# Performance work log

Measured on AMD Instinct MI355X. Metric: run time of the kernel, lower is better.

## Reference

```python
import jax, jax.numpy as jnp
import numpy as np

D_MODEL = 1024
NUM_HEADS = 16
D_K = D_MODEL // NUM_HEADS
CLAMP = 1e9
EPS = 1e-12


def setup_inputs() -> dict:
    key = jax.random.key(0)
    ks = jax.random.split(key, 11)
    B, S, D = 4, 2048, D_MODEL
    std = 1.0 / np.sqrt(D)
    inp = {
        'Q': jax.random.normal(ks[0], (B, S, D), jnp.float32),
        'K': jax.random.normal(ks[1], (B, S, D), jnp.float32),
        'V': jax.random.normal(ks[2], (B, S, D), jnp.float32),
        'Wq': jax.random.normal(ks[3], (D, D), jnp.float32) * std,
        'bq': jnp.zeros((D,), jnp.float32),
        'Wk': jax.random.normal(ks[4], (D, D), jnp.float32) * std,
        'bk': jnp.zeros((D,), jnp.float32),
        'Wv': jax.random.normal(ks[5], (D, D), jnp.float32) * std,
        'bv': jnp.zeros((D,), jnp.float32),
        'Wo': jax.random.normal(ks[6], (D, D), jnp.float32) * std,
        'bo': jnp.zeros((D,), jnp.float32),
    }
    return inp


def _split_heads(x):
    b, s, _ = x.shape
    return x.reshape(b, s, NUM_HEADS, D_K).transpose(0, 2, 1, 3)  # [b,h,s,dk]


def reference(Q, K, V, Wq, bq, Wk, bk, Wv, bv, Wo, bo):
    Qh = _split_heads(Q @ Wq.T + bq)
    Kh = _split_heads(K @ Wk.T + bk)
    Vh = _split_heads(V @ Wv.T + bv)
    scale = jnp.sqrt(jnp.asarray(D_K, Qh.dtype))
    scores = jnp.einsum('bhqd,bhkd->bhqk', Qh, Kh) / scale
    scores = scores - jnp.max(scores, axis=-1, keepdims=True)
    scores = jnp.clip(scores, -CLAMP, CLAMP)
    attn = jax.nn.softmax(scores, axis=-1)
    attn = jnp.clip(attn, EPS, None)
    attn = attn / jnp.sum(attn, axis=-1, keepdims=True)
    ctx = jnp.einsum('bhqk,bhkd->bhqd', attn, Vh)
    b, h, s, dk = ctx.shape
    ctx = ctx.transpose(0, 2, 1, 3).reshape(b, s, D_MODEL)
    return ctx @ Wo.T + bo
```

## Files before the change

### kernel.cpp

```cpp
#include <hip/hip_runtime.h>
#include <hip/hip_bf16.h>


typedef float  f32x4  __attribute__((ext_vector_type(4)));
typedef __bf16 bf16x8 __attribute__((ext_vector_type(8)));
typedef short  s16x8  __attribute__((ext_vector_type(8)));

#define MFMA16(a,b,c) __builtin_amdgcn_mfma_f32_16x16x32_bf16((a),(b),(c),0,0,0)

__device__ __forceinline__ unsigned short f2bf(float f) {
    union { float f; unsigned u; } v; v.f = f;
    unsigned r = v.u + 0x7fffu + ((v.u >> 16) & 1u);
    return (unsigned short)(r >> 16);
}

__device__ __forceinline__ s16x8 cvt8(const float* __restrict__ p) {
    f32x4 x = *(const f32x4*)p;
    f32x4 y = *(const f32x4*)(p + 4);
    s16x8 r;
    r[0] = (short)f2bf(x[0]); r[1] = (short)f2bf(x[1]);
    r[2] = (short)f2bf(x[2]); r[3] = (short)f2bf(x[3]);
    r[4] = (short)f2bf(y[0]); r[5] = (short)f2bf(y[1]);
    r[6] = (short)f2bf(y[2]); r[7] = (short)f2bf(y[3]);
    return r;
}

__device__ __forceinline__ void gl_lds16(const void* g, void* l) {
    __builtin_amdgcn_global_load_lds(
        (const __attribute__((address_space(1))) unsigned int*)g,
        (__attribute__((address_space(3))) unsigned int*)l, 16, 0, 0);
}

__global__ __launch_bounds__(256) void cvt_kernel(
    const float* __restrict__ src, unsigned short* __restrict__ dst, int n8)
{
    int i = blockIdx.x * 256 + threadIdx.x;
    if (i < n8) *(s16x8*)(dst + (size_t)i * 8) = cvt8(src + (size_t)i * 8);
}

template <int MODE>
__global__ __launch_bounds__(256) void gemm_bf16(
    const unsigned short* __restrict__ A,
    const unsigned short* __restrict__ W,
    const float* __restrict__ bias,
    void* __restrict__ Cv)
{
    constexpr int K = 1024;
    __shared__ unsigned short Ash[128 * 32];
    __shared__ unsigned short Bsh[128 * 32];

    const int t    = threadIdx.x;
    const int w    = t >> 6;
    const int lane = t & 63;
    const int wm   = w >> 1, wn = w & 1;
    const int lr   = lane & 15, quad = lane >> 4;

    const int m0 = blockIdx.y * 128;
    const int n0 = blockIdx.x * 128;

    const int srow = t >> 2;
    const int skp  = (t & 3) * 8;

    const unsigned short* Ap0 = A + (size_t)(m0 + srow) * K + skp;
    const unsigned short* Ap1 = Ap0 + (size_t)64 * K;
    const unsigned short* Wp0 = W + (size_t)(n0 + srow) * K + skp;
    const unsigned short* Wp1 = Wp0 + (size_t)64 * K;
    unsigned short* lA0 = &Ash[w * 512];
    unsigned short* lA1 = &Ash[2048 + w * 512];
    unsigned short* lB0 = &Bsh[w * 512];
    unsigned short* lB1 = &Bsh[2048 + w * 512];

    f32x4 acc[4][4] = {};

    for (int k0 = 0; k0 < K; k0 += 32) {
        __syncthreads();
        gl_lds16(Ap0 + k0, lA0);
        gl_lds16(Ap1 + k0, lA1);
        gl_lds16(Wp0 + k0, lB0);
        gl_lds16(Wp1 + k0, lB1);
        __syncthreads();

        bf16x8 af[4], bw[4];
#pragma unroll
        for (int i = 0; i < 4; i++)
            af[i] = *(const bf16x8*)&Ash[(wm * 64 + i * 16 + lr) * 32 + quad * 8];
#pragma unroll
        for (int j = 0; j < 4; j++)
            bw[j] = *(const bf16x8*)&Bsh[(wn * 64 + j * 16 + lr) * 32 + quad * 8];

#pragma unroll
        for (int i = 0; i < 4; i++)
#pragma unroll
            for (int j = 0; j < 4; j++)
                acc[i][j] = MFMA16(af[i], bw[j], acc[i][j]);
    }

#pragma unroll
    for (int i = 0; i < 4; i++) {
#pragma unroll
        for (int j = 0; j < 4; j++) {
            const int n = n0 + wn * 64 + j * 16 + lr;
#pragma unroll
            for (int r = 0; r < 4; r++) {
                const int m = m0 + wm * 64 + i * 16 + quad * 4 + r;
                float val = acc[i][j][r] + ((MODE == 2) ? bias[m] : bias[n]);
                if (MODE == 0) {
                    const int b = m >> 11, s = m & 2047, h = n >> 6, d = n & 63;
                    ((unsigned short*)Cv)[(((size_t)(b * 16 + h) * 2048 + s) << 6) + d] = f2bf(val);
                } else if (MODE == 1) {
                    ((float*)Cv)[(size_t)m * 1024 + n] = val;
                } else {
                    const int h = m >> 6, d = m & 63, b = n >> 11, s = n & 2047;
                    ((unsigned short*)Cv)[((size_t)(b * 16 + h) * 64 + d) * 2048 + s] = f2bf(val);
                }
            }
        }
    }
}

__global__ __launch_bounds__(256) void attn_kernel(
    const unsigned short* __restrict__ Qh,
    const unsigned short* __restrict__ Kh,
    const unsigned short* __restrict__ Vt,
    unsigned short* __restrict__ ctx)
{
    constexpr int KS = 72;
    __shared__ unsigned short Ksh[64 * KS];
    __shared__ unsigned short Vts[64 * KS];
    __shared__ unsigned short Psh[4][16 * KS];

    const int t    = threadIdx.x;
    const int w    = t >> 6;
    const int lane = t & 63;
    const int lr   = lane & 15, quad = lane >> 4;

    const int bh = blockIdx.y, qblk = blockIdx.x;
    const size_t base = (size_t)bh * 2048 * 64;
    const unsigned short* Qp = Qh + base;
    const unsigned short* Kg = Kh + base + (size_t)lane * 64 + w * 16;
    const unsigned short* Vg = Vt + base + (size_t)lane * 2048 + w * 16;

    const int q0 = qblk * 64 + w * 16;
    bf16x8 aq0 = *(const bf16x8*)(Qp + (size_t)(q0 + lr) * 64 + quad * 8);
    bf16x8 aq1 = *(const bf16x8*)(Qp + (size_t)(q0 + lr) * 64 + 32 + quad * 8);

    f32x4 Of[4] = {};
    float lsum[4] = {0.f, 0.f, 0.f, 0.f};

    for (int kb = 0; kb < 2048; kb += 64) {
        s16x8 kv0 = *(const s16x8*)(Kg + (size_t)kb * 64);
        s16x8 kv1 = *(const s16x8*)(Kg + (size_t)kb * 64 + 8);
        s16x8 vv0 = *(const s16x8*)(Vg + kb);
        s16x8 vv1 = *(const s16x8*)(Vg + kb + 8);

        __syncthreads();
        *(s16x8*)&Ksh[lane * KS + w * 16]     = kv0;
        *(s16x8*)&Ksh[lane * KS + w * 16 + 8] = kv1;
        *(s16x8*)&Vts[lane * KS + w * 16]     = vv0;
        *(s16x8*)&Vts[lane * KS + w * 16 + 8] = vv1;
        __syncthreads();

        f32x4 sc[4];
#pragma unroll
        for (int nt = 0; nt < 4; nt++) {
            const unsigned short* kr = &Ksh[(16 * nt + lr) * KS + quad * 8];
            f32x4 c = {};
            c = MFMA16(aq0, *(const bf16x8*)kr, c);
            c = MFMA16(aq1, *(const bf16x8*)(kr + 32), c);
            sc[nt] = c;
        }

#pragma unroll
        for (int r = 0; r < 4; r++) {
            float p0 = __expf(sc[0][r] * 0.125f);
            float p1 = __expf(sc[1][r] * 0.125f);
            float p2 = __expf(sc[2][r] * 0.125f);
            float p3 = __expf(sc[3][r] * 0.125f);
            lsum[r] += (p0 + p1) + (p2 + p3);
            unsigned short* pr = &Psh[w][(quad * 4 + r) * KS + lr];
            pr[0]  = f2bf(p0);
            pr[16] = f2bf(p1);
            pr[32] = f2bf(p2);
            pr[48] = f2bf(p3);
        }
        __asm__ __volatile__("s_waitcnt lgkmcnt(0)" ::: "memory");

        bf16x8 pf0 = *(const bf16x8*)&Psh[w][lr * KS + quad * 8];
        bf16x8 pf1 = *(const bf16x8*)&Psh[w][lr * KS + 32 + quad * 8];
#pragma unroll
        for (int dt = 0; dt < 4; dt++) {
            const unsigned short* vr = &Vts[(dt * 16 + lr) * KS + quad * 8];
            Of[dt] = MFMA16(pf0, *(const bf16x8*)vr, Of[dt]);
            Of[dt] = MFMA16(pf1, *(const bf16x8*)(vr + 32), Of[dt]);
        }
    }

    const int b = bh >> 4, h = bh & 15;
#pragma unroll
    for (int r = 0; r < 4; r++) {
        float l = lsum[r];
        l += __shfl_xor(l, 1);
        l += __shfl_xor(l, 2);
        l += __shfl_xor(l, 4);
        l += __shfl_xor(l, 8);
        const float inv = 1.0f / l;
        const int q = q0 + quad * 4 + r;
        unsigned short* cp = ctx + ((size_t)b * 2048 + q) * 1024 + h * 64;
#pragma unroll
        for (int dt = 0; dt < 4; dt++)
            cp[dt * 16 + lr] = f2bf(Of[dt][r] * inv);
    }
}

extern "C" void kernel_launch(void* const* d_in, const int* in_sizes, int n_in,
                              void* d_out, int out_size, void* d_ws, size_t ws_size,
                              hipStream_t stream) {
    const float* Q  = (const float*)d_in[0];
    const float* K  = (const float*)d_in[1];
    const float* V  = (const float*)d_in[2];
    const float* Wq = (const float*)d_in[3];
    const float* bq = (const float*)d_in[4];
    const float* Wk = (const float*)d_in[5];
    const float* bk = (const float*)d_in[6];
    const float* Wv = (const float*)d_in[7];
    const float* bv = (const float*)d_in[8];
    const float* Wo = (const float*)d_in[9];
    const float* bo = (const float*)d_in[10];

    const size_t EB = (size_t)8192 * 1024;
    const size_t EW = (size_t)1024 * 1024;
    unsigned short* Xb  = (unsigned short*)d_ws;
    unsigned short* Wqb = Xb  + EB;
    unsigned short* Wkb = Wqb + EW;
    unsigned short* Wvb = Wkb + EW;
    unsigned short* Wob = Wvb + EW;
    unsigned short* Qh  = Wob + EW;
    unsigned short* Kh  = Qh  + EB;
    unsigned short* Vtw = Kh  + EB;
    unsigned short* Ctx = Xb;

    const int n8b = (int)(EB / 8);
    const int n8w = (int)(EW / 8);

    cvt_kernel<<<n8w / 256, 256, 0, stream>>>(Wq, Wqb, n8w);
    cvt_kernel<<<n8w / 256, 256, 0, stream>>>(Wk, Wkb, n8w);
    cvt_kernel<<<n8w / 256, 256, 0, stream>>>(Wv, Wvb, n8w);
    cvt_kernel<<<n8w / 256, 256, 0, stream>>>(Wo, Wob, n8w);

    dim3 tb(256), gP(8, 64), gT(64, 8);

    cvt_kernel<<<n8b / 256, 256, 0, stream>>>(Q, Xb, n8b);
    gemm_bf16<0><<<gP, tb, 0, stream>>>(Xb, Wqb, bq, Qh);

    cvt_kernel<<<n8b / 256, 256, 0, stream>>>(K, Xb, n8b);
    gemm_bf16<0><<<gP, tb, 0, stream>>>(Xb, Wkb, bk, Kh);

    cvt_kernel<<<n8b / 256, 256, 0, stream>>>(V, Xb, n8b);
    gemm_bf16<2><<<gT, tb, 0, stream>>>(Wvb, Xb, bv, Vtw);

    attn_kernel<<<dim3(32, 64), tb, 0, stream>>>(Qh, Kh, Vtw, Ctx);

    gemm_bf16<1><<<gP, tb, 0, stream>>>(Ctx, Wob, bo, (float*)d_out);
}
```

Measured before the change: 435.3 us.

## Keep softmax probabilities in registers via transposed QK MFMA and permlane swaps

Swaps the operand order of the QK^T MFMA so the score tile comes out transposed, with each lane holding scores for a single query across keys. The probabilities are then packed to bf16 with v_cvt_pk_bf16_f32 and rearranged with permlane32/16 swaps into the A-operand layout for the PV MFMA. This removes the per-wave LDS round trip for P (bf16 stores, waitcnt, reloads) and the manual bf16 rounding. Row sums are reduced with cross-quad shuffles and broadcast at the end. It relies on gfx950-specific instructions and on the permlane mapping being correct.

```diff
diff --git a/kernel.cpp b/kernel.cpp
--- a/kernel.cpp
+++ b/kernel.cpp
@@ -5,6 +5,7 @@
 typedef float  f32x4  __attribute__((ext_vector_type(4)));
 typedef __bf16 bf16x8 __attribute__((ext_vector_type(8)));
 typedef short  s16x8  __attribute__((ext_vector_type(8)));
+typedef int    i32x4  __attribute__((ext_vector_type(4)));
 
 #define MFMA16(a,b,c) __builtin_amdgcn_mfma_f32_16x16x32_bf16((a),(b),(c),0,0,0)
 
@@ -29,6 +30,18 @@
     __builtin_amdgcn_global_load_lds(
         (const __attribute__((address_space(1))) unsigned int*)g,
         (__attribute__((address_space(3))) unsigned int*)l, 16, 0, 0);
+}
+
+__device__ __forceinline__ int cvtpk_bf16(float lo, float hi) {
+    int r;
+    asm("v_cvt_pk_bf16_f32 %0, %1, %2" : "=v"(r) : "v"(lo), "v"(hi));
+    return r;
+}
+__device__ __forceinline__ void plswap32(int& a, int& b) {
+    asm("v_permlane32_swap_b32 %0, %1" : "+v"(a), "+v"(b));
+}
+__device__ __forceinline__ void plswap16(int& a, int& b) {
+    asm("v_permlane16_swap_b32 %0, %1" : "+v"(a), "+v"(b));
 }
 
 __global__ __launch_bounds__(256) void cvt_kernel(
@@ -127,7 +140,6 @@
     constexpr int KS = 72;
     __shared__ unsigned short Ksh[64 * KS];
     __shared__ unsigned short Vts[64 * KS];
-    __shared__ unsigned short Psh[4][16 * KS];
 
     const int t    = threadIdx.x;
     const int w    = t >> 6;
@@ -145,7 +157,7 @@
     bf16x8 aq1 = *(const bf16x8*)(Qp + (size_t)(q0 + lr) * 64 + 32 + quad * 8);
 
     f32x4 Of[4] = {};
-    float lsum[4] = {0.f, 0.f, 0.f, 0.f};
+    float lsum = 0.f;
 
     for (int kb = 0; kb < 2048; kb += 64) {
         s16x8 kv0 = *(const s16x8*)(Kg + (size_t)kb * 64);
@@ -160,33 +172,39 @@
         *(s16x8*)&Vts[lane * KS + w * 16 + 8] = vv1;
         __syncthreads();
 
-        f32x4 sc[4];
+        f32x4 pe[4];
 #pragma unroll
         for (int nt = 0; nt < 4; nt++) {
             const unsigned short* kr = &Ksh[(16 * nt + lr) * KS + quad * 8];
             f32x4 c = {};
-            c = MFMA16(aq0, *(const bf16x8*)kr, c);
-            c = MFMA16(aq1, *(const bf16x8*)(kr + 32), c);
-            sc[nt] = c;
+            c = MFMA16(*(const bf16x8*)kr, aq0, c);
+            c = MFMA16(*(const bf16x8*)(kr + 32), aq1, c);
+            f32x4 p;
+#pragma unroll
+            for (int r = 0; r < 4; r++) p[r] = __expf(c[r] * 0.125f);
+            lsum += (p[0] + p[1]) + (p[2] + p[3]);
+            pe[nt] = p;
         }
 
-#pragma unroll
-        for (int r = 0; r < 4; r++) {
-            float p0 = __expf(sc[0][r] * 0.125f);
-            float p1 = __expf(sc[1][r] * 0.125f);
-            float p2 = __expf(sc[2][r] * 0.125f);
-            float p3 = __expf(sc[3][r] * 0.125f);
-            lsum[r] += (p0 + p1) + (p2 + p3);
-            unsigned short* pr = &Psh[w][(quad * 4 + r) * KS + lr];
-            pr[0]  = f2bf(p0);
-            pr[16] = f2bf(p1);
-            pr[32] = f2bf(p2);
-            pr[48] = f2bf(p3);
-        }
-        __asm__ __volatile__("s_waitcnt lgkmcnt(0)" ::: "memory");
-
-        bf16x8 pf0 = *(const bf16x8*)&Psh[w][lr * KS + quad * 8];
-        bf16x8 pf1 = *(const bf16x8*)&Psh[w][lr * KS + 32 + quad * 8];
+        int a0 = cvtpk_bf16(pe[0][0], pe[0][1]);
+        int a1 = cvtpk_bf16(pe[0][2], pe[0][3]);
+        int b0 = cvtpk_bf16(pe[1][0], pe[1][1]);
+        int b1 = cvtpk_bf16(pe[1][2], pe[1][3]);
+        plswap32(a0, b0); plswap32(a1, b1);
+        plswap16(a0, b0); plswap16(a1, b1);
+        i32x4 f0; f0[0] = a0; f0[1] = a1; f0[2] = b0; f0[3] = b1;
+
+        int c0 = cvtpk_bf16(pe[2][0], pe[2][1]);
+        int c1 = cvtpk_bf16(pe[2][2], pe[2][3]);
+        int d0 = cvtpk_bf16(pe[3][0], pe[3][1]);
+        int d1 = cvtpk_bf16(pe[3][2], pe[3][3]);
+        plswap32(c0, d0); plswap32(c1, d1);
+        plswap16(c0, d0); plswap16(c1, d1);
+        i32x4 f1; f1[0] = c0; f1[1] = c1; f1[2] = d0; f1[3] = d1;
+
+        bf16x8 pf0 = __builtin_bit_cast(bf16x8, f0);
+        bf16x8 pf1 = __builtin_bit_cast(bf16x8, f1);
+
 #pragma unroll
         for (int dt = 0; dt < 4; dt++) {
             const unsigned short* vr = &Vts[(dt * 16 + lr) * KS + quad * 8];
@@ -195,15 +213,13 @@
         }
     }
 
+    lsum += __shfl_xor(lsum, 16);
+    lsum += __shfl_xor(lsum, 32);
+
     const int b = bh >> 4, h = bh & 15;
 #pragma unroll
     for (int r = 0; r < 4; r++) {
-        float l = lsum[r];
-        l += __shfl_xor(l, 1);
-        l += __shfl_xor(l, 2);
-        l += __shfl_xor(l, 4);
-        l += __shfl_xor(l, 8);
-        const float inv = 1.0f / l;
+        const float inv = 1.0f / __shfl(lsum, quad * 4 + r, 64);
         const int q = q0 + quad * 4 + r;
         unsigned short* cp = ctx + ((size_t)b * 2048 + q) * 1024 + h * 64;
 #pragma unroll
```

New measurement: 458.2 us. 5.3% more time.
